# Kernel tuning notes

Hardware: AMD Instinct MI355X
Metric: run time of the kernel (lower is better)

The kernel has to match this reference:

```python
import jax, jax.numpy as jnp
import numpy as np

UNITS = 1024
D = 1024

def setup_inputs() -> dict:
    key = jax.random.key(0)
    ks = jax.random.split(key, 8)
    B, T = 32, 2048
    query = jax.random.normal(ks[0], (B, D), dtype=jnp.float32)
    values = jax.random.normal(ks[1], (B, T, D), dtype=jnp.float32)
    s1 = 1.0 / np.sqrt(D)
    s2 = 1.0 / np.sqrt(UNITS)
    W1 = jax.random.normal(ks[2], (D, UNITS), dtype=jnp.float32) * s1
    b1 = jnp.zeros((UNITS,), dtype=jnp.float32)
    W2 = jax.random.normal(ks[3], (D, UNITS), dtype=jnp.float32) * s1
    b2 = jnp.zeros((UNITS,), dtype=jnp.float32)
    Wv = jax.random.normal(ks[4], (UNITS, 1), dtype=jnp.float32) * s2
    bv = jnp.zeros((1,), dtype=jnp.float32)
    return {"query": query, "values": values, "W1": W1, "b1": b1,
            "W2": W2, "b2": b2, "Wv": Wv, "bv": bv}

def reference(query, values, W1, b1, W2, b2, Wv, bv):
    # query: [B, D]; values: [B, T, D]
    q_proj = query @ W1 + b1                     # [B, U]
    v_proj = jnp.einsum('btd,du->btu', values, W2) + b2  # [B, T, U]
    h = jnp.tanh(q_proj[:, None, :] + v_proj)    # [B, T, U]
    score = jnp.einsum('btu,uo->bto', h, Wv) + bv  # [B, T, 1]
    attention_weights = jax.nn.softmax(score, axis=1)  # [B, T, 1]
    context_vector = jnp.sum(attention_weights * values, axis=1)  # [B, D]
    return (context_vector, attention_weights)
```

## Files before the change

### kernel.cpp

```cpp
#include <hip/hip_runtime.h>
#include <hip/hip_bf16.h>
#include <stdint.h>


typedef unsigned short ushort_t;
typedef short bf16x8 __attribute__((ext_vector_type(8)));
typedef float f32x4 __attribute__((ext_vector_type(4)));

#define GLOBAL_AS __attribute__((address_space(1)))
#define LDS_AS    __attribute__((address_space(3)))

__device__ __forceinline__ ushort_t f2bf(float f) {
    union { float f; unsigned int u; } v;
    v.f = f;
    unsigned int u = v.u;
    unsigned int r = u + 0x7FFFu + ((u >> 16) & 1u);
    return (ushort_t)(r >> 16);
}
__device__ __forceinline__ unsigned int pk2(float a, float b) {
    union { __hip_bfloat162 h; unsigned int u; } c;
    c.h = __float22bfloat162_rn(make_float2(a, b));
    return c.u;
}
__device__ __forceinline__ float fast_tanh(float x) {
    float ax = __builtin_fabsf(x);
    float e = __expf(-2.0f * ax);
    float t = (1.0f - e) * __builtin_amdgcn_rcpf(1.0f + e);
    return __builtin_copysignf(t, x);
}

static constexpr int B_ = 32, T_ = 2048, D_ = 1024, U_ = 1024;
static constexpr int M_ = B_ * T_;
static constexpr int TRANS_B = 1024;
static constexpr int QPROJ_B = 64;
static constexpr int CONV_B  = 4096;

__global__ __launch_bounds__(256) void k_prep(const float* __restrict__ W2,
                                              const float* __restrict__ query,
                                              const float* __restrict__ W1,
                                              const float* __restrict__ b1,
                                              const float* __restrict__ b2,
                                              const float* __restrict__ values,
                                              ushort_t* __restrict__ W2T,
                                              float* __restrict__ qpb,
                                              ushort_t* __restrict__ vb,
                                              unsigned int* __restrict__ cnt) {
    __shared__ float smem[8192 + 4 * 64 * 9];
    int bid = blockIdx.x;
    const int tid = threadIdx.x;

    if (bid < TRANS_B) {
        if (bid == 0 && tid < B_) cnt[tid] = 0u;
        float(*tile)[33] = (float(*)[33])smem;
        int u0 = (bid & 31) * 32, d0 = (bid >> 5) * 32;
        int tx = tid & 31, ty = tid >> 5;
#pragma unroll
        for (int r = 0; r < 4; ++r)
            tile[ty + r * 8][tx] = W2[(size_t)(d0 + ty + r * 8) * U_ + (u0 + tx)];
        __syncthreads();
#pragma unroll
        for (int r = 0; r < 4; ++r)
            W2T[(size_t)(u0 + ty + r * 8) * D_ + (d0 + tx)] = f2bf(tile[tx][ty + r * 8]);
        return;
    }
    bid -= TRANS_B;

    if (bid >= QPROJ_B) {
        const int cb = bid - QPROJ_B;
        const size_t base = (size_t)cb * 2048 + tid;
#pragma unroll
        for (int k = 0; k < 8; ++k) {
            const size_t chunk = base + (size_t)k * 256;
            const float* s = values + chunk * 8;
            f32x4 v0 = *(const f32x4*)s;
            f32x4 v1 = *(const f32x4*)(s + 4);
            uint4 p;
            p.x = pk2(v0[0], v0[1]);
            p.y = pk2(v0[2], v0[3]);
            p.z = pk2(v1[0], v1[1]);
            p.w = pk2(v1[2], v1[3]);
            *(uint4*)(vb + chunk * 8) = p;
        }
        return;
    }

    const int bg = bid >> 4;
    const int uc = bid & 15;

    float* qs = smem;
    float(*red)[64][9] = (float(*)[64][9])(smem + 8192);

    for (int i = tid; i < 8 * 1024; i += 256)
        qs[i] = query[(size_t)(bg * 8 + (i >> 10)) * D_ + (i & 1023)];
    __syncthreads();

    const int ul = tid & 63, ds = tid >> 6;
    const int u = uc * 64 + ul;
    float acc[8] = {0.f, 0.f, 0.f, 0.f, 0.f, 0.f, 0.f, 0.f};
#pragma unroll 8
    for (int d = ds * 256; d < ds * 256 + 256; ++d) {
        const float w = W1[(size_t)d * U_ + u];
#pragma unroll
        for (int b = 0; b < 8; ++b) acc[b] += qs[(b << 10) + d] * w;
    }
#pragma unroll
    for (int b = 0; b < 8; ++b) red[ds][ul][b] = acc[b];
    __syncthreads();
    for (int i = tid; i < 512; i += 256) {
        const int b = i & 7, uu = i >> 3;
        const float s = (red[0][uu][b] + red[1][uu][b]) + (red[2][uu][b] + red[3][uu][b]);
        const int ug = uc * 64 + uu;
        qpb[(size_t)(bg * 8 + b) * U_ + ug] = s + b1[ug] + b2[ug];
    }
}

#define BM 128
#define BN 128
#define BK 64

__global__ __launch_bounds__(256) void k_score_gemm(const ushort_t* __restrict__ vb,
                                                    const ushort_t* __restrict__ W2T,
                                                    const float* __restrict__ qpb,
                                                    const float* __restrict__ Wv,
                                                    float* __restrict__ scores_partial) {
    __shared__ ushort_t As[BM * BK];
    __shared__ ushort_t Bs[BN * BK];
    __shared__ float sScore[BM];

    const int tid = threadIdx.x;
    const int lane = tid & 63;
    const int w = tid >> 6;
    const int wm = w >> 1, wn = w & 1;

    const int g = blockIdx.x;
    const int mt = ((g >> 6) << 3) | (g & 7);
    const int nt = (g >> 3) & 7;
    const int m0 = mt * BM, n0 = nt * BN;

    if (tid < BM) sScore[tid] = 0.f;

    f32x4 acc[4][4];
#pragma unroll
    for (int i = 0; i < 4; ++i)
#pragma unroll
        for (int j = 0; j < 4; ++j) acc[i][j] = (f32x4){0.f, 0.f, 0.f, 0.f};

    const int lr = lane >> 3;
    const int cS = (lane & 7) ^ lr;
    const ushort_t* bBase = W2T + (size_t)(n0 + w * 8 + lr) * D_ + cS * 8;
    const ushort_t* aBase = vb + (size_t)(m0 + w * 8 + lr) * D_ + cS * 8;

    const int quad = lane >> 4;
    const int l15 = lane & 15;
    const int l7 = l15 & 7;

    for (int k0 = 0; k0 < D_; k0 += BK) {
#pragma unroll
        for (int i = 0; i < 4; ++i) {
            __builtin_amdgcn_global_load_lds(
                (const GLOBAL_AS void*)(bBase + k0 + (size_t)i * 32 * D_),
                (LDS_AS void*)(Bs + i * 2048 + w * 512), 16, 0, 0);
        }
#pragma unroll
        for (int i = 0; i < 4; ++i) {
            __builtin_amdgcn_global_load_lds(
                (const GLOBAL_AS void*)(aBase + k0 + (size_t)i * 32 * D_),
                (LDS_AS void*)(As + i * 2048 + w * 512), 16, 0, 0);
        }
        __syncthreads();
#pragma unroll
        for (int kk = 0; kk < BK; kk += 32) {
            bf16x8 af[4], bfr[4];
            const int cb = kk >> 3;
#pragma unroll
            for (int i = 0; i < 4; ++i) {
                int r = wm * 64 + i * 16 + l15;
                af[i] = *(const bf16x8*)(As + (r << 6) + (((quad + cb) ^ l7) << 3));
            }
#pragma unroll
            for (int j = 0; j < 4; ++j) {
                int r = wn * 64 + j * 16 + l15;
                bfr[j] = *(const bf16x8*)(Bs + (r << 6) + (((quad + cb) ^ l7) << 3));
            }
#pragma unroll
            for (int i = 0; i < 4; ++i)
#pragma unroll
                for (int j = 0; j < 4; ++j)
                    acc[i][j] = __builtin_amdgcn_mfma_f32_16x16x32_bf16(
                        af[i], bfr[j], acc[i][j], 0, 0, 0);
        }
        __syncthreads();
    }

    const int b = m0 >> 11;
    const float* qp = qpb + b * U_;
    float qv[4], wv[4];
#pragma unroll
    for (int j = 0; j < 4; ++j) {
        int u = n0 + wn * 64 + j * 16 + l15;
        qv[j] = qp[u];
        wv[j] = Wv[u];
    }
#pragma unroll
    for (int i = 0; i < 4; ++i) {
#pragma unroll
        for (int r = 0; r < 4; ++r) {
            float s = 0.f;
#pragma unroll
            for (int j = 0; j < 4; ++j) s += fast_tanh(acc[i][j][r] + qv[j]) * wv[j];
            s += __shfl_xor(s, 1);
            s += __shfl_xor(s, 2);
            s += __shfl_xor(s, 4);
            s += __shfl_xor(s, 8);
            if (l15 == 0) atomicAdd(&sScore[wm * 64 + i * 16 + quad * 4 + r], s);
        }
    }
    __syncthreads();
    if (tid < BM) scores_partial[(size_t)(m0 + tid) * 8 + nt] = sScore[tid];
}

__global__ __launch_bounds__(256) void k_smax_ctx(const float* __restrict__ scores_partial,
                                                  const float* __restrict__ bv,
                                                  const float* __restrict__ values,
                                                  float* __restrict__ ctx_part,
                                                  unsigned int* __restrict__ cnt,
                                                  float* __restrict__ out_w,
                                                  float* __restrict__ out_ctx) {
    const int tc = blockIdx.x;
    const int b = blockIdx.y;
    const int tid = threadIdx.x;
    __shared__ float s[T_];
    __shared__ float red[4];
    __shared__ float wls[128];
    __shared__ unsigned int is_last;
    const float bvf = bv[0];

    float lmax = -1e30f;
    for (int t = tid; t < T_; t += 256) {
        const float* p = scores_partial + (size_t)(b * T_ + t) * 8;
        float sc = ((p[0] + p[1]) + (p[2] + p[3])) + ((p[4] + p[5]) + (p[6] + p[7])) + bvf;
        s[t] = sc;
        lmax = fmaxf(lmax, sc);
    }
    for (int off = 32; off; off >>= 1) lmax = fmaxf(lmax, __shfl_xor(lmax, off));
    if ((tid & 63) == 0) red[tid >> 6] = lmax;
    __syncthreads();
    const float gmax = fmaxf(fmaxf(red[0], red[1]), fmaxf(red[2], red[3]));

    float lsum = 0.f;
    for (int t = tid; t < T_; t += 256) {
        float e = __expf(s[t] - gmax);
        s[t] = e;
        lsum += e;
    }
    for (int off = 32; off; off >>= 1) lsum += __shfl_xor(lsum, off);
    __syncthreads();
    if ((tid & 63) == 0) red[tid >> 6] = lsum;
    __syncthreads();
    const float ginv = 1.f / ((red[0] + red[1]) + (red[2] + red[3]));

    if (tid < 128) {
        float wgt = s[tc * 128 + tid] * ginv;
        wls[tid] = wgt;
        out_w[b * T_ + tc * 128 + tid] = wgt;
    }
    __syncthreads();

    f32x4 acc = (f32x4){0.f, 0.f, 0.f, 0.f};
    const float* base = values + (size_t)(b * T_ + tc * 128) * D_ + tid * 4;
#pragma unroll 4
    for (int tt = 0; tt < 128; ++tt)
        acc += wls[tt] * *(const f32x4*)(base + (size_t)tt * D_);
    *(f32x4*)(ctx_part + ((size_t)(tc * 32 + b) << 10) + tid * 4) = acc;

    __threadfence();
    if (tid == 0) is_last = (atomicAdd(&cnt[b], 1u) == 15u) ? 1u : 0u;
    __syncthreads();
    if (is_last) {
        __threadfence();
        f32x4 ssum = (f32x4){0.f, 0.f, 0.f, 0.f};
#pragma unroll
        for (int q = 0; q < 16; ++q)
            ssum += *(const f32x4*)(ctx_part + ((size_t)(q * 32 + b) << 10) + tid * 4);
        *(f32x4*)(out_ctx + b * D_ + tid * 4) = ssum;
        if (tid == 0) cnt[b] = 0u;
    }
}

extern "C" void kernel_launch(void* const* d_in, const int* in_sizes, int n_in,
                              void* d_out, int out_size, void* d_ws, size_t ws_size,
                              hipStream_t stream) {
    const float* query  = (const float*)d_in[0];
    const float* values = (const float*)d_in[1];
    const float* W1     = (const float*)d_in[2];
    const float* b1     = (const float*)d_in[3];
    const float* W2     = (const float*)d_in[4];
    const float* b2     = (const float*)d_in[5];
    const float* Wv     = (const float*)d_in[6];
    const float* bv     = (const float*)d_in[7];

    float* out_ctx = (float*)d_out;
    float* out_w   = out_ctx + B_ * D_;

    char* ws = (char*)d_ws;
    const size_t OFF_W2T = 0;
    const size_t OFF_QPB = 0x200000;
    const size_t OFF_SP  = 0x220000;
    const size_t OFF_CNT = 0x420000;
    const size_t OFF_VB  = 0x500000;

    ushort_t*     W2T            = (ushort_t*)(ws + OFF_W2T);
    float*        ctx_part       = (float*)(ws + OFF_W2T);
    float*        qpb            = (float*)(ws + OFF_QPB);
    float*        scores_partial = (float*)(ws + OFF_SP);
    unsigned int* cnt            = (unsigned int*)(ws + OFF_CNT);
    ushort_t*     vb             = (ushort_t*)(ws + OFF_VB);

    k_prep<<<dim3(TRANS_B + QPROJ_B + CONV_B), 256, 0, stream>>>(
        W2, query, W1, b1, b2, values, W2T, qpb, vb, cnt);
    k_score_gemm<<<dim3((M_ / BM) * (U_ / BN)), 256, 0, stream>>>(
        vb, W2T, qpb, Wv, scores_partial);
    k_smax_ctx<<<dim3(16, B_), 256, 0, stream>>>(
        scores_partial, bv, values, ctx_part, cnt, out_w, out_ctx);

    (void)in_sizes; (void)n_in; (void)out_size; (void)ws_size;
}
```

Baseline: 703.1 us.

## Split softmax/context kernel into three kernels and reorder prep block roles

The fused softmax+context kernel, which recomputed the full softmax in each of 16 blocks per batch and used an atomic last-block reduction, becomes three kernels. A single softmax kernel per batch writes the weights, a context kernel with 32 T-chunks per batch reads them, and a finishing kernel sums the partials. The prep kernel's block order is changed so the q-projection blocks come first and the W2 transpose last, and the counter reset is dropped. This removes redundant softmax work and the atomics and threadfences, but adds two kernel launches and an extra pass over the weights.

```diff
diff --git a/kernel.cpp b/kernel.cpp
--- a/kernel.cpp
+++ b/kernel.cpp
@@ -31,9 +31,9 @@
 
 static constexpr int B_ = 32, T_ = 2048, D_ = 1024, U_ = 1024;
 static constexpr int M_ = B_ * T_;
-static constexpr int TRANS_B = 1024;
 static constexpr int QPROJ_B = 64;
 static constexpr int CONV_B  = 4096;
+static constexpr int TRANS_B = 1024;
 
 __global__ __launch_bounds__(256) void k_prep(const float* __restrict__ W2,
                                               const float* __restrict__ query,
@@ -43,31 +43,47 @@
                                               const float* __restrict__ values,
                                               ushort_t* __restrict__ W2T,
                                               float* __restrict__ qpb,
-                                              ushort_t* __restrict__ vb,
-                                              unsigned int* __restrict__ cnt) {
+                                              ushort_t* __restrict__ vb) {
     __shared__ float smem[8192 + 4 * 64 * 9];
     int bid = blockIdx.x;
     const int tid = threadIdx.x;
 
-    if (bid < TRANS_B) {
-        if (bid == 0 && tid < B_) cnt[tid] = 0u;
-        float(*tile)[33] = (float(*)[33])smem;
-        int u0 = (bid & 31) * 32, d0 = (bid >> 5) * 32;
-        int tx = tid & 31, ty = tid >> 5;
-#pragma unroll
-        for (int r = 0; r < 4; ++r)
-            tile[ty + r * 8][tx] = W2[(size_t)(d0 + ty + r * 8) * U_ + (u0 + tx)];
-        __syncthreads();
-#pragma unroll
-        for (int r = 0; r < 4; ++r)
-            W2T[(size_t)(u0 + ty + r * 8) * D_ + (d0 + tx)] = f2bf(tile[tx][ty + r * 8]);
+    if (bid < QPROJ_B) {
+        const int bg = bid >> 4;
+        const int uc = bid & 15;
+
+        float* qs = smem;
+        float(*red)[64][9] = (float(*)[64][9])(smem + 8192);
+
+        for (int i = tid; i < 8 * 1024; i += 256)
+            qs[i] = query[(size_t)(bg * 8 + (i >> 10)) * D_ + (i & 1023)];
+        __syncthreads();
+
+        const int ul = tid & 63, ds = tid >> 6;
+        const int u = uc * 64 + ul;
+        float acc[8] = {0.f, 0.f, 0.f, 0.f, 0.f, 0.f, 0.f, 0.f};
+#pragma unroll 8
+        for (int d = ds * 256; d < ds * 256 + 256; ++d) {
+            const float w = W1[(size_t)d * U_ + u];
+#pragma unroll
+            for (int b = 0; b < 8; ++b) acc[b] += qs[(b << 10) + d] * w;
+        }
+#pragma unroll
+        for (int b = 0; b < 8; ++b) red[ds][ul][b] = acc[b];
+        __syncthreads();
+        for (int i = tid; i < 512; i += 256) {
+            const int b = i & 7, uu = i >> 3;
+            const float s =
+                (red[0][uu][b] + red[1][uu][b]) + (red[2][uu][b] + red[3][uu][b]);
+            const int ug = uc * 64 + uu;
+            qpb[(size_t)(bg * 8 + b) * U_ + ug] = s + b1[ug] + b2[ug];
+        }
         return;
     }
-    bid -= TRANS_B;
-
-    if (bid >= QPROJ_B) {
-        const int cb = bid - QPROJ_B;
-        const size_t base = (size_t)cb * 2048 + tid;
+    bid -= QPROJ_B;
+
+    if (bid < CONV_B) {
+        const size_t base = (size_t)bid * 2048 + tid;
 #pragma unroll
         for (int k = 0; k < 8; ++k) {
             const size_t chunk = base + (size_t)k * 256;
@@ -83,34 +99,19 @@
         }
         return;
     }
-
-    const int bg = bid >> 4;
-    const int uc = bid & 15;
-
-    float* qs = smem;
-    float(*red)[64][9] = (float(*)[64][9])(smem + 8192);
-
-    for (int i = tid; i < 8 * 1024; i += 256)
-        qs[i] = query[(size_t)(bg * 8 + (i >> 10)) * D_ + (i & 1023)];
-    __syncthreads();
-
-    const int ul = tid & 63, ds = tid >> 6;
-    const int u = uc * 64 + ul;
-    float acc[8] = {0.f, 0.f, 0.f, 0.f, 0.f, 0.f, 0.f, 0.f};
-#pragma unroll 8
-    for (int d = ds * 256; d < ds * 256 + 256; ++d) {
-        const float w = W1[(size_t)d * U_ + u];
-#pragma unroll
-        for (int b = 0; b < 8; ++b) acc[b] += qs[(b << 10) + d] * w;
-    }
-#pragma unroll
-    for (int b = 0; b < 8; ++b) red[ds][ul][b] = acc[b];
-    __syncthreads();
-    for (int i = tid; i < 512; i += 256) {
-        const int b = i & 7, uu = i >> 3;
-        const float s = (red[0][uu][b] + red[1][uu][b]) + (red[2][uu][b] + red[3][uu][b]);
-        const int ug = uc * 64 + uu;
-        qpb[(size_t)(bg * 8 + b) * U_ + ug] = s + b1[ug] + b2[ug];
+    bid -= CONV_B;
+
+    {
+        float(*tile)[33] = (float(*)[33])smem;
+        int u0 = (bid & 31) * 32, d0 = (bid >> 5) * 32;
+        int tx = tid & 31, ty = tid >> 5;
+#pragma unroll
+        for (int r = 0; r < 4; ++r)
+            tile[ty + r * 8][tx] = W2[(size_t)(d0 + ty + r * 8) * U_ + (u0 + tx)];
+        __syncthreads();
+#pragma unroll
+        for (int r = 0; r < 4; ++r)
+            W2T[(size_t)(u0 + ty + r * 8) * D_ + (d0 + tx)] = f2bf(tile[tx][ty + r * 8]);
     }
 }
 
@@ -219,20 +220,13 @@
     if (tid < BM) scores_partial[(size_t)(m0 + tid) * 8 + nt] = sScore[tid];
 }
 
-__global__ __launch_bounds__(256) void k_smax_ctx(const float* __restrict__ scores_partial,
-                                                  const float* __restrict__ bv,
-                                                  const float* __restrict__ values,
-                                                  float* __restrict__ ctx_part,
-                                                  unsigned int* __restrict__ cnt,
-                                                  float* __restrict__ out_w,
-                                                  float* __restrict__ out_ctx) {
-    const int tc = blockIdx.x;
-    const int b = blockIdx.y;
-    const int tid = threadIdx.x;
+__global__ __launch_bounds__(256) void k_softmax(const float* __restrict__ scores_partial,
+                                                 const float* __restrict__ bv,
+                                                 float* __restrict__ out_w) {
+    const int b = blockIdx.x;
     __shared__ float s[T_];
     __shared__ float red[4];
-    __shared__ float wls[128];
-    __shared__ unsigned int is_last;
+    const int tid = threadIdx.x;
     const float bvf = bv[0];
 
     float lmax = -1e30f;
@@ -259,32 +253,36 @@
     __syncthreads();
     const float ginv = 1.f / ((red[0] + red[1]) + (red[2] + red[3]));
 
-    if (tid < 128) {
-        float wgt = s[tc * 128 + tid] * ginv;
-        wls[tid] = wgt;
-        out_w[b * T_ + tc * 128 + tid] = wgt;
-    }
+    for (int t = tid; t < T_; t += 256) out_w[b * T_ + t] = s[t] * ginv;
+}
+
+__global__ __launch_bounds__(256) void k_ctx(const float* __restrict__ values,
+                                             const float* __restrict__ out_w,
+                                             float* __restrict__ ctx_part) {
+    const int tc = blockIdx.x;
+    const int b = blockIdx.y;
+    const int tid = threadIdx.x;
+    __shared__ float wls[64];
+    if (tid < 64) wls[tid] = out_w[b * T_ + tc * 64 + tid];
     __syncthreads();
 
     f32x4 acc = (f32x4){0.f, 0.f, 0.f, 0.f};
-    const float* base = values + (size_t)(b * T_ + tc * 128) * D_ + tid * 4;
+    const float* base = values + (size_t)(b * T_ + tc * 64) * D_ + tid * 4;
 #pragma unroll 4
-    for (int tt = 0; tt < 128; ++tt)
+    for (int tt = 0; tt < 64; ++tt)
         acc += wls[tt] * *(const f32x4*)(base + (size_t)tt * D_);
     *(f32x4*)(ctx_part + ((size_t)(tc * 32 + b) << 10) + tid * 4) = acc;
-
-    __threadfence();
-    if (tid == 0) is_last = (atomicAdd(&cnt[b], 1u) == 15u) ? 1u : 0u;
-    __syncthreads();
-    if (is_last) {
-        __threadfence();
-        f32x4 ssum = (f32x4){0.f, 0.f, 0.f, 0.f};
-#pragma unroll
-        for (int q = 0; q < 16; ++q)
-            ssum += *(const f32x4*)(ctx_part + ((size_t)(q * 32 + b) << 10) + tid * 4);
-        *(f32x4*)(out_ctx + b * D_ + tid * 4) = ssum;
-        if (tid == 0) cnt[b] = 0u;
-    }
+}
+
+__global__ __launch_bounds__(256) void k_ctx_fin(const float* __restrict__ ctx_part,
+                                                 float* __restrict__ out_ctx) {
+    const int b = blockIdx.x;
+    const int tid = threadIdx.x;
+    f32x4 s = (f32x4){0.f, 0.f, 0.f, 0.f};
+#pragma unroll
+    for (int tc = 0; tc < 32; ++tc)
+        s += *(const f32x4*)(ctx_part + ((size_t)(tc * 32 + b) << 10) + tid * 4);
+    *(f32x4*)(out_ctx + b * D_ + tid * 4) = s;
 }
 
 extern "C" void kernel_launch(void* const* d_in, const int* in_sizes, int n_in,
@@ -306,22 +304,21 @@
     const size_t OFF_W2T = 0;
     const size_t OFF_QPB = 0x200000;
     const size_t OFF_SP  = 0x220000;
-    const size_t OFF_CNT = 0x420000;
     const size_t OFF_VB  = 0x500000;
 
-    ushort_t*     W2T            = (ushort_t*)(ws + OFF_W2T);
-    float*        ctx_part       = (float*)(ws + OFF_W2T);
-    float*        qpb            = (float*)(ws + OFF_QPB);
-    float*        scores_partial = (float*)(ws + OFF_SP);
-    unsigned int* cnt            = (unsigned int*)(ws + OFF_CNT);
-    ushort_t*     vb             = (ushort_t*)(ws + OFF_VB);
-
-    k_prep<<<dim3(TRANS_B + QPROJ_B + CONV_B), 256, 0, stream>>>(
-        W2, query, W1, b1, b2, values, W2T, qpb, vb, cnt);
+    ushort_t* W2T            = (ushort_t*)(ws + OFF_W2T);
+    float*    ctx_part       = (float*)(ws + OFF_W2T);
+    float*    qpb            = (float*)(ws + OFF_QPB);
+    float*    scores_partial = (float*)(ws + OFF_SP);
+    ushort_t* vb             = (ushort_t*)(ws + OFF_VB);
+
+    k_prep<<<dim3(QPROJ_B + CONV_B + TRANS_B), 256, 0, stream>>>(
+        W2, query, W1, b1, b2, values, W2T, qpb, vb);
     k_score_gemm<<<dim3((M_ / BM) * (U_ / BN)), 256, 0, stream>>>(
         vb, W2T, qpb, Wv, scores_partial);
-    k_smax_ctx<<<dim3(16, B_), 256, 0, stream>>>(
-        scores_partial, bv, values, ctx_part, cnt, out_w, out_ctx);
+    k_softmax<<<dim3(B_), 256, 0, stream>>>(scores_partial, bv, out_w);
+    k_ctx<<<dim3(32, B_), 256, 0, stream>>>(values, out_w, ctx_part);
+    k_ctx_fin<<<dim3(B_), 256, 0, stream>>>(ctx_part, out_ctx);
 
     (void)in_sizes; (void)n_in; (void)out_size; (void)ws_size;
 }
```

Measured after the change: 628.5 us. -10.6%, faster.
